# Kernel tuning notes

Measured on AMD Instinct MI355X. Metric: run time of the kernel, lower is better.

Reference implementation:

```python
import jax, jax.numpy as jnp
import numpy as np

KSIZE = 3
ALPHA = 1.0
BETA = 1.0


def _cubic(t):
    # torch bicubic kernel, a = -0.75
    a = -0.75
    t = jnp.abs(t)
    return jnp.where(
        t <= 1.0,
        (a + 2.0) * t**3 - (a + 3.0) * t**2 + 1.0,
        jnp.where(t < 2.0, a * t**3 - 5.0 * a * t**2 + 8.0 * a * t - 4.0 * a, 0.0),
    )


def _resize1d(x, axis, out_size):
    # bicubic, align_corners=False (src = (dst+0.5)*scale - 0.5), clamped border indices
    in_size = x.shape[axis]
    scale = in_size / out_size
    coords = (jnp.arange(out_size, dtype=x.dtype) + 0.5) * scale - 0.5
    base = jnp.floor(coords).astype(jnp.int32)
    offs = jnp.arange(-1, 3)
    idx = jnp.clip(base[:, None] + offs[None, :], 0, in_size - 1)          # [out,4]
    w = _cubic(coords[:, None] - (base[:, None] + offs[None, :]).astype(x.dtype))  # [out,4]
    xm = jnp.moveaxis(x, axis, -1)
    g = xm[..., idx]                                                        # [...,out,4]
    out = jnp.einsum('...of,of->...o', g, w)
    return jnp.moveaxis(out, -1, axis)


def bicubic_resize(img, out_h, out_w):
    return _resize1d(_resize1d(img, 2, out_h), 3, out_w)


def compute_patches(x, k):
    # x: [B,3,H,W] -> non-overlapping k x k patches -> 3x3 gram per patch -> [B,Np,9]
    B, C, H, W = x.shape
    p = x.reshape(B, C, H // k, k, W // k, k)
    p = p.transpose(0, 2, 4, 1, 3, 5).reshape(B, -1, C, k * k)  # [B,Np,3,k*k]
    G = jnp.einsum('bpci,bpdi->bpcd', p, p) / (C * k * k)        # [B,Np,3,3]
    return G.reshape(B, -1, C * C)


def batch_pairwise_distance_l2(x, y):
    # squared euclidean: [B,N,D] x [B,M,D] -> [B,N,M]
    x2 = jnp.sum(x * x, axis=-1)[:, :, None]
    y2 = jnp.sum(y * y, axis=-1)[:, None, :]
    return x2 + y2 - 2.0 * jnp.einsum('bnd,bmd->bnm', x, y)


def setup_inputs() -> dict:
    key = jax.random.key(0)
    k1, k2 = jax.random.split(key)
    x = jax.random.uniform(k1, (8, 3, 144, 144), dtype=jnp.float32)
    gt = jax.random.uniform(k2, (8, 3, 144, 144), dtype=jnp.float32)
    return {"x": x, "gt": gt}


def reference(x, gt):
    k = KSIZE
    B, C, H, W = gt.shape
    p1 = compute_patches(x, k)                       # [B,N,9]
    p2 = compute_patches(gt, k)                      # [B,N,9]
    gt_2 = bicubic_resize(gt, H // 2, W // 2)
    gt_4 = bicubic_resize(gt, H // 4, W // 4)
    p2_cat = jnp.concatenate(
        [p2, compute_patches(gt_2, k), compute_patches(gt_4, k)], axis=1)  # [B,M,9]
    score = ALPHA * batch_pairwise_distance_l2(p1, p2_cat) \
          + BETA * batch_pairwise_distance_l2(p2, p2_cat)                  # [B,N,M]
    ind = jnp.argmin(score, axis=2)                                        # [B,N]
    sel_p2 = jnp.take_along_axis(p2_cat, ind[:, :, None], axis=1)          # [B,N,9]
    return jnp.mean(jnp.abs(p1 - sel_p2))
```

## Files before the change

kernel.cpp:

```cpp
#include <hip/hip_runtime.h>
#include <math.h>

#define NB 8
#define NC 3
#define HH 144
#define WW 144
#define NPAT 2304
#define NPTOT (NB * NPAT)
#define MCAT 3024
#define MCATP 3072
#define SPLITS 2
#define CSPLIT 1536
#define CHUNK 512
#define ROUNDS 3
#define STEPS 2
#define PPT 6
#define WAVES 4
#define PPB (PPT * WAVES)
#define BLOCKS_PER_B (NPAT / PPB)
#define NBLK_SCORE (NB * BLOCKS_PER_B * SPLITS)
#define NBLK_MERGE (NPTOT / 256)

typedef float f4 __attribute__((ext_vector_type(4)));

__device__ __forceinline__ int iclamp(int v, int lo, int hi) {
    return v < lo ? lo : (v > hi ? hi : v);
}

__device__ __forceinline__ float to_sgpr(float v) {
    return __int_as_float(__builtin_amdgcn_readfirstlane(__float_as_int(v)));
}

__global__ void resize_all(const float* __restrict__ gt,
                           float* __restrict__ gt2, float* __restrict__ gt4) {
    const int T2 = NB * NC * 72 * 72;
    const int T4 = NB * NC * 36 * 36;
    int idx = blockIdx.x * blockDim.x + threadIdx.x;
    if (idx >= T2 + T4) return;
    int scale, HO, WO;
    float* dst;
    int li;
    if (idx < T2) { scale = 2; HO = 72; WO = 72; dst = gt2; li = idx; }
    else          { scale = 4; HO = 36; WO = 36; dst = gt4; li = idx - T2; }
    int w  = li % WO;
    int h  = (li / WO) % HO;
    int bc = li / (WO * HO);
    const float* G = gt + (size_t)bc * HH * WW;
    int tr = scale * h + (scale >> 1) - 2;
    int tc = scale * w + (scale >> 1) - 2;
    int r0 = iclamp(tr + 0, 0, HH - 1) * WW;
    int r1 = iclamp(tr + 1, 0, HH - 1) * WW;
    int r2 = iclamp(tr + 2, 0, HH - 1) * WW;
    int r3 = iclamp(tr + 3, 0, HH - 1) * WW;
    float acc = 0.0f;
#pragma unroll
    for (int cc = 0; cc < 4; cc++) {
        int col = iclamp(tc + cc, 0, WW - 1);
        float hv = 0.0f;
        hv += -0.09375f * G[r0 + col];
        hv +=  0.59375f * G[r1 + col];
        hv +=  0.59375f * G[r2 + col];
        hv += -0.09375f * G[r3 + col];
        float wt = (cc == 0 || cc == 3) ? -0.09375f : 0.59375f;
        acc += wt * hv;
    }
    dst[li] = acc;
}

__device__ __forceinline__ void patch_gram(const float* __restrict__ src, int H, int W,
                                           int b, int n, float* __restrict__ g) {
    int PW = W / 3;
    int ph = n / PW, pw = n % PW;
    float p[3][9];
#pragma unroll
    for (int c = 0; c < 3; c++) {
        const float* s = src + ((size_t)b * NC + c) * H * W + (size_t)(ph * 3) * W + pw * 3;
#pragma unroll
        for (int i = 0; i < 3; i++)
#pragma unroll
            for (int j = 0; j < 3; j++)
                p[c][i * 3 + j] = s[i * W + j];
    }
#pragma unroll
    for (int c = 0; c < 3; c++)
#pragma unroll
        for (int e = 0; e < 3; e++) {
            float s = 0.0f;
#pragma unroll
            for (int q = 0; q < 9; q++) s += p[c][q] * p[e][q];
            g[c * 3 + e] = s / 27.0f;
        }
}

__device__ __forceinline__ void store_cand(float* __restrict__ p2cT, int b, int m,
                                           const float g[9]) {
    float y2 = 0.0f;
#pragma unroll
    for (int j = 0; j < 9; j++) {
        p2cT[((size_t)b * 10 + j) * MCATP + m] = g[j];
        y2 += g[j] * g[j];
    }
    p2cT[((size_t)b * 10 + 9) * MCATP + m] = 2.0f * y2;
}

__global__ void patch_all(const float* __restrict__ x, const float* __restrict__ gt,
                          const float* __restrict__ gt2, const float* __restrict__ gt4,
                          float* __restrict__ p1, float* __restrict__ p2cT,
                          float* __restrict__ pw) {
    const int R0 = NPTOT;
    const int R1 = NB * 576;
    const int R2 = NB * 144;
    int idx = blockIdx.x * blockDim.x + threadIdx.x;
    if (idx >= R0 + R1 + R2 + NB * 48) return;

    if (idx < R0) {
        int b = idx / NPAT, n = idx % NPAT;
        float g1[9], g2[9];
        patch_gram(x,  144, 144, b, n, g1);
        patch_gram(gt, 144, 144, b, n, g2);
        float* d = p1 + (size_t)idx * 9;
#pragma unroll
        for (int j = 0; j < 9; j++) d[j] = g1[j];
        store_cand(p2cT, b, n, g2);
        float* W = pw + (size_t)idx * 12;
#pragma unroll
        for (int j = 0; j < 9; j++) W[j] = -2.0f * (g1[j] + g2[j]);
        W[9]  = 0.0f;
        W[10] = 0.0f;
        W[11] = 0.0f;
        return;
    }
    if (idx < R0 + R1) {
        int li = idx - R0;
        int b = li / 576, n = li % 576;
        float g[9];
        patch_gram(gt2, 72, 72, b, n, g);
        store_cand(p2cT, b, NPAT + n, g);
        return;
    }
    if (idx < R0 + R1 + R2) {
        int li = idx - R0 - R1;
        int b = li / 144, n = li % 144;
        float g[9];
        patch_gram(gt4, 36, 36, b, n, g);
        store_cand(p2cT, b, NPAT + 576 + n, g);
        return;
    }
    {
        int li = idx - R0 - R1 - R2;
        int b = li / 48, m = MCAT + li % 48;
#pragma unroll
        for (int j = 0; j < 9; j++) p2cT[((size_t)b * 10 + j) * MCATP + m] = 0.0f;
        p2cT[((size_t)b * 10 + 9) * MCATP + m] = 1e30f;
    }
}

__global__ __launch_bounds__(256) void score_kernel(const float* __restrict__ p2cT,
                                                    const float* __restrict__ pw,
                                                    float* __restrict__ best_s,
                                                    int* __restrict__ best_i) {
    __shared__ float candT[10][CHUNK];

    int t     = threadIdx.x;
    int lane  = t & 63;
    int wv    = t >> 6;
    int blk   = blockIdx.x;
    int b     = blk / (SPLITS * BLOCKS_PER_B);
    int r     = blk % (SPLITS * BLOCKS_PER_B);
    int split = r / BLOCKS_PER_B;
    int bb    = r % BLOCKS_PER_B;
    int nbase = bb * PPB + wv * PPT;

    const float* PB = p2cT + (size_t)b * 10 * MCATP;

    float aa2[PPT][9];
#pragma unroll
    for (int p = 0; p < PPT; p++) {
        const float* W = pw + (size_t)(b * NPAT + nbase + p) * 12;
#pragma unroll
        for (int j = 0; j < 9; j++) aa2[p][j] = to_sgpr(W[j]);
    }

    float best[PPT];
    int   besti[PPT];
#pragma unroll
    for (int p = 0; p < PPT; p++) { best[p] = INFINITY; besti[p] = 0x7fffffff; }

#pragma unroll 1
    for (int rd = 0; rd < ROUNDS; rd++) {
        int cb = split * CSPLIT + rd * CHUNK;
#pragma unroll 1
        for (int i = t; i < 10 * (CHUNK / 4); i += 256) {
            int plane = i >> 7, c4 = i & 127;
            *(f4*)&candT[plane][c4 * 4] = *(const f4*)&PB[(size_t)plane * MCATP + cb + c4 * 4];
        }
        __syncthreads();

#pragma unroll
        for (int st = 0; st < STEPS; st++) {
            int cl = st * 256 + lane * 4;
            f4 T4 = *(const f4*)&candT[9][cl];
            f4 s4[PPT];
#pragma unroll
            for (int p = 0; p < PPT; p++) s4[p] = T4;
#pragma unroll
            for (int j = 0; j < 9; j++) {
                f4 v4 = *(const f4*)&candT[j][cl];
#pragma unroll
                for (int p = 0; p < PPT; p++) s4[p] += aa2[p][j] * v4;
            }
            int cg = cb + cl;
#pragma unroll
            for (int p = 0; p < PPT; p++) {
                if (s4[p].x < best[p]) { best[p] = s4[p].x; besti[p] = cg + 0; }
                if (s4[p].y < best[p]) { best[p] = s4[p].y; besti[p] = cg + 1; }
                if (s4[p].z < best[p]) { best[p] = s4[p].z; besti[p] = cg + 2; }
                if (s4[p].w < best[p]) { best[p] = s4[p].w; besti[p] = cg + 3; }
            }
        }
        __syncthreads();
    }

#pragma unroll
    for (int p = 0; p < PPT; p++) {
#pragma unroll
        for (int m = 1; m < 64; m <<= 1) {
            float ob = __shfl_xor(best[p], m);
            int   oi = __shfl_xor(besti[p], m);
            if (ob < best[p] || (ob == best[p] && oi < besti[p])) { best[p] = ob; besti[p] = oi; }
        }
        if (lane == 0) {
            size_t o = (size_t)split * NPTOT + (size_t)b * NPAT + nbase + p;
            best_s[o] = best[p];
            best_i[o] = besti[p];
        }
    }
}

__global__ __launch_bounds__(256) void merge_kernel(const float* __restrict__ p1,
                                                    const float* __restrict__ p2cT,
                                                    const float* __restrict__ best_s,
                                                    const int* __restrict__ best_i,
                                                    float* __restrict__ parts) {
    __shared__ float wsum[4];
    int t  = threadIdx.x;
    int gp = blockIdx.x * 256 + t;
    int b  = gp / NPAT;
    float s0 = best_s[gp];
    int   i0 = best_i[gp];
    float s1 = best_s[NPTOT + gp];
    int   i1 = best_i[NPTOT + gp];
    int bi = (s1 < s0) ? i1 : i0;
    const float* P1 = p1 + (size_t)gp * 9;
    const float* PB = p2cT + (size_t)b * 10 * MCATP;
    float l = 0.0f;
#pragma unroll
    for (int j = 0; j < 9; j++) l += fabsf(P1[j] - PB[(size_t)j * MCATP + bi]);
#pragma unroll
    for (int m = 1; m < 64; m <<= 1) l += __shfl_xor(l, m);
    if ((t & 63) == 0) wsum[t >> 6] = l;
    __syncthreads();
    if (t == 0) parts[blockIdx.x] = (wsum[0] + wsum[1]) + (wsum[2] + wsum[3]);
}

__global__ void final_kernel(const float* __restrict__ parts, float* __restrict__ out) {
    int lane = threadIdx.x;
    float s = 0.0f;
    for (int i = lane; i < NBLK_MERGE; i += 64) s += parts[i];
#pragma unroll
    for (int m = 1; m < 64; m <<= 1) s += __shfl_xor(s, m);
    if (lane == 0) out[0] = s / 165888.0f;
}

extern "C" void kernel_launch(void* const* d_in, const int* in_sizes, int n_in,
                              void* d_out, int out_size, void* d_ws, size_t ws_size,
                              hipStream_t stream) {
    const float* x  = (const float*)d_in[0];
    const float* gt = (const float*)d_in[1];
    float* out = (float*)d_out;

    float* ws     = (float*)d_ws;
    float* gt2    = ws;
    float* gt4    = gt2  + NB * NC * 72 * 72;
    float* p1     = gt4  + NB * NC * 36 * 36;
    float* p2cT   = p1 + (size_t)NPTOT * 9;
    float* pw     = p2cT + (size_t)NB * 10 * MCATP;
    float* best_s = pw + (size_t)NPTOT * 12;
    int*   best_i = (int*)(best_s + SPLITS * NPTOT);
    float* parts  = (float*)(best_i + SPLITS * NPTOT);

    {
        int tot = NB * NC * 72 * 72 + NB * NC * 36 * 36;
        resize_all<<<(tot + 255) / 256, 256, 0, stream>>>(gt, gt2, gt4);
    }
    {
        int tot = NPTOT + NB * 576 + NB * 144 + NB * 48;
        patch_all<<<(tot + 255) / 256, 256, 0, stream>>>(x, gt, gt2, gt4, p1, p2cT, pw);
    }
    score_kernel<<<NBLK_SCORE, 256, 0, stream>>>(p2cT, pw, best_s, best_i);
    merge_kernel<<<NBLK_MERGE, 256, 0, stream>>>(p1, p2cT, best_s, best_i, parts);
    final_kernel<<<1, 64, 0, stream>>>(parts, out);
}
```

Measured before the change: 57.07 us.

## Read candidate planes directly from global memory instead of staging in LDS

The score kernel no longer copies candidate chunks into shared memory with block-wide barriers. Each wave now reads two candidates per lane straight from global memory (float2) across twelve steps covering its 1536-candidate split. This removes the LDS staging, the __syncthreads, and the LDS footprint, which could raise occupancy. In exchange, every wave fetches the same candidate data from global/L2, which adds cache traffic, and the narrower per-lane vector means more load instructions.

```diff
diff --git a/kernel.cpp b/kernel.cpp
--- a/kernel.cpp
+++ b/kernel.cpp
@@ -11,9 +11,7 @@
 #define MCATP 3072
 #define SPLITS 2
 #define CSPLIT 1536
-#define CHUNK 512
-#define ROUNDS 3
-#define STEPS 2
+#define STEPS 12
 #define PPT 6
 #define WAVES 4
 #define PPB (PPT * WAVES)
@@ -21,7 +19,7 @@
 #define NBLK_SCORE (NB * BLOCKS_PER_B * SPLITS)
 #define NBLK_MERGE (NPTOT / 256)
 
-typedef float f4 __attribute__((ext_vector_type(4)));
+typedef float f2 __attribute__((ext_vector_type(2)));
 
 __device__ __forceinline__ int iclamp(int v, int lo, int hi) {
     return v < lo ? lo : (v > hi ? hi : v);
@@ -159,8 +157,6 @@
                                                     const float* __restrict__ pw,
                                                     float* __restrict__ best_s,
                                                     int* __restrict__ best_i) {
-    __shared__ float candT[10][CHUNK];
-
     int t     = threadIdx.x;
     int lane  = t & 63;
     int wv    = t >> 6;
@@ -186,39 +182,25 @@
 #pragma unroll
     for (int p = 0; p < PPT; p++) { best[p] = INFINITY; besti[p] = 0x7fffffff; }
 
+    int cb = split * CSPLIT;
 #pragma unroll 1
-    for (int rd = 0; rd < ROUNDS; rd++) {
-        int cb = split * CSPLIT + rd * CHUNK;
-#pragma unroll 1
-        for (int i = t; i < 10 * (CHUNK / 4); i += 256) {
-            int plane = i >> 7, c4 = i & 127;
-            *(f4*)&candT[plane][c4 * 4] = *(const f4*)&PB[(size_t)plane * MCATP + cb + c4 * 4];
-        }
-        __syncthreads();
-
-#pragma unroll
-        for (int st = 0; st < STEPS; st++) {
-            int cl = st * 256 + lane * 4;
-            f4 T4 = *(const f4*)&candT[9][cl];
-            f4 s4[PPT];
-#pragma unroll
-            for (int p = 0; p < PPT; p++) s4[p] = T4;
-#pragma unroll
-            for (int j = 0; j < 9; j++) {
-                f4 v4 = *(const f4*)&candT[j][cl];
-#pragma unroll
-                for (int p = 0; p < PPT; p++) s4[p] += aa2[p][j] * v4;
-            }
-            int cg = cb + cl;
-#pragma unroll
-            for (int p = 0; p < PPT; p++) {
-                if (s4[p].x < best[p]) { best[p] = s4[p].x; besti[p] = cg + 0; }
-                if (s4[p].y < best[p]) { best[p] = s4[p].y; besti[p] = cg + 1; }
-                if (s4[p].z < best[p]) { best[p] = s4[p].z; besti[p] = cg + 2; }
-                if (s4[p].w < best[p]) { best[p] = s4[p].w; besti[p] = cg + 3; }
-            }
-        }
-        __syncthreads();
+    for (int st = 0; st < STEPS; st++) {
+        int cl = cb + st * 128 + lane * 2;
+        f2 Tv = *(const f2*)&PB[(size_t)9 * MCATP + cl];
+        f2 s[PPT];
+#pragma unroll
+        for (int p = 0; p < PPT; p++) s[p] = Tv;
+#pragma unroll
+        for (int j = 0; j < 9; j++) {
+            f2 v = *(const f2*)&PB[(size_t)j * MCATP + cl];
+#pragma unroll
+            for (int p = 0; p < PPT; p++) s[p] += aa2[p][j] * v;
+        }
+#pragma unroll
+        for (int p = 0; p < PPT; p++) {
+            if (s[p].x < best[p]) { best[p] = s[p].x; besti[p] = cl; }
+            if (s[p].y < best[p]) { best[p] = s[p].y; besti[p] = cl + 1; }
+        }
     }
 
 #pragma unroll
```

Measured after the change: 50.17 us (median of 2 runs). -12.1%, faster.
